# Optimization experiments

Measured on AMD Instinct MI355X. Metric: run time of the kernel, lower is better.

## Reference

```python
import jax, jax.numpy as jnp
import numpy as np

# Complete 32-ary tree of depth 3: vocab = 32**3 = 32768 leaves.
B = 4096       # batch
NHID = 512     # hidden size
BR = 32        # branching factor (num_children at every internal node)
DEPTH = 3      # number of internal-node decisions from root to leaf
V = BR ** DEPTH
NUM_NODES = sum(BR ** k for k in range(DEPTH))  # 1 + 32 + 1024 = 1057

# Static tree-indexing tables (level-order node numbering).
_LEVEL_OFFSET = np.array([sum(BR ** j for j in range(k)) for k in range(DEPTH)], dtype=np.int64)   # [0, 1, 33]
_NODE_DIV = np.array([BR ** (DEPTH - k) for k in range(DEPTH)], dtype=np.int64)                    # node-within-level divisor
_STEP_DIV = np.array([BR ** (DEPTH - 1 - k) for k in range(DEPTH)], dtype=np.int64)                # child-step divisor


def setup_inputs() -> dict:
    key = jax.random.key(0)
    k1, k2, k3 = jax.random.split(key, 3)
    inputs = jax.random.normal(k1, (B, NHID), dtype=jnp.float32)
    labels = jax.random.randint(k2, (B,), 0, V)                     # leaf index per sample
    W = jax.random.normal(k3, (NUM_NODES, NHID, BR), dtype=jnp.float32)  # all node params, stacked
    return {"inputs": inputs, "labels": labels, "W": W}


def reference(inputs, labels, W):
    lab = labels[:, None]                                            # [B, 1]
    node_idx = jnp.asarray(_LEVEL_OFFSET)[None, :] + lab // jnp.asarray(_NODE_DIV)[None, :]  # [B, D] node on path
    steps = (lab // jnp.asarray(_STEP_DIV)[None, :]) % BR            # [B, D] child taken at each node
    Wg = W[node_idx]                                                 # [B, D, NHID, BR] gathered path params
    logits = jnp.einsum('bh,bdhc->bdc', inputs, Wg)                  # [B, D, BR]
    p = jax.nn.softmax(logits, axis=-1)
    step_p = jnp.take_along_axis(p, steps[:, :, None], axis=-1)[..., 0]  # [B, D]
    return jnp.prod(step_p, axis=-1)                                 # [B] path probability
```

## Files before the change

### kernel.cpp

```cpp
#include <hip/hip_runtime.h>


#define NHID  512
#define BR    32
#define BATCH 4096
#define NBUCK 1024
#define SMAX  4
#define SCAP  64

__device__ __forceinline__ float dpp_xadd1(float v) {
    int m = __builtin_amdgcn_update_dpp(0, __float_as_int(v), 0xB1, 0xF, 0xF, true);
    return v + __int_as_float(m);
}
__device__ __forceinline__ float dpp_xadd2(float v) {
    int m = __builtin_amdgcn_update_dpp(0, __float_as_int(v), 0x4E, 0xF, 0xF, true);
    return v + __int_as_float(m);
}

#define FMA4(A, xv, wv_) do { \
    (A).x = fmaf((xv), (wv_).x, (A).x); \
    (A).y = fmaf((xv), (wv_).y, (A).y); \
    (A).z = fmaf((xv), (wv_).z, (A).z); \
    (A).w = fmaf((xv), (wv_).w, (A).w); } while (0)

__global__ __launch_bounds__(256, 4) void hsm_fused(
    const float* __restrict__ inputs,
    const int* __restrict__ labels,
    const float* __restrict__ W,
    float* __restrict__ out)
{
    __shared__ float xsT[NHID * SMAX];
    __shared__ float partial[8 * 3 * SMAX * BR];
    __shared__ float pk[3][SMAX];
    __shared__ int   slist[SCAP];
    __shared__ int   scount;

    const int g   = blockIdx.x;
    const int tid = threadIdx.x;

    if (tid == 0) scount = 0;
    __syncthreads();

    #pragma unroll
    for (int r = 0; r < BATCH / 256; ++r) {
        int j = tid + 256 * r;
        int lab = labels[j];
        if ((lab >> 5) == g) {
            int p = atomicAdd(&scount, 1);
            if (p < SCAP) slist[p] = (j << 5) | (lab & 31);
        }
    }
    __syncthreads();
    const int n = min(scount, SCAP);
    if (n == 0) return;

    const int wv   = tid >> 6;
    const int lane = tid & 63;
    const int hsel = lane & 7;
    const int colg = lane >> 3;

    const int node1 = 1 + (g >> 5);
    const int node2 = 33 + g;

    const size_t laneoff = (size_t)wv * 1024 + hsel * 8 + colg;
    const float4* wp0 = (const float4*)W + laneoff;
    const float4* wp1 = (const float4*)(W + (size_t)node1 * (NHID * BR)) + laneoff;
    const float4* wp2 = (const float4*)(W + (size_t)node2 * (NHID * BR)) + laneoff;
    const float4* xs4 = (const float4*)xsT;

    for (int c0 = 0; c0 < n; c0 += SMAX) {
        const int m = min(SMAX, n - c0);

        __syncthreads();
        #pragma unroll
        for (int r = 0; r < 2; ++r) {
            int h = tid + 256 * r;
            float v[SMAX];
            #pragma unroll
            for (int s = 0; s < SMAX; ++s) {
                float x = 0.0f;
                if (s < m) {
                    int sid = slist[c0 + s] >> 5;
                    x = inputs[(size_t)sid * NHID + h];
                }
                v[s] = x;
            }
            ((float4*)xsT)[h] = make_float4(v[0], v[1], v[2], v[3]);
        }
        __syncthreads();

        float4 acc[3][SMAX];
        #pragma unroll
        for (int k = 0; k < 3; ++k)
            #pragma unroll
            for (int s = 0; s < SMAX; ++s) acc[k][s] = make_float4(0, 0, 0, 0);

        #pragma unroll 4
        for (int i = 0; i < 16; ++i) {
            float4 w0 = wp0[i * 64];
            float4 w1 = wp1[i * 64];
            float4 w2 = wp2[i * 64];
            float4 x4 = xs4[wv * 128 + i * 8 + hsel];
            FMA4(acc[0][0], x4.x, w0); FMA4(acc[0][1], x4.y, w0);
            FMA4(acc[0][2], x4.z, w0); FMA4(acc[0][3], x4.w, w0);
            FMA4(acc[1][0], x4.x, w1); FMA4(acc[1][1], x4.y, w1);
            FMA4(acc[1][2], x4.z, w1); FMA4(acc[1][3], x4.w, w1);
            FMA4(acc[2][0], x4.x, w2); FMA4(acc[2][1], x4.y, w2);
            FMA4(acc[2][2], x4.z, w2); FMA4(acc[2][3], x4.w, w2);
        }

        #pragma unroll
        for (int k = 0; k < 3; ++k) {
            #pragma unroll
            for (int s = 0; s < SMAX; ++s) {
                acc[k][s].x = dpp_xadd2(dpp_xadd1(acc[k][s].x));
                acc[k][s].y = dpp_xadd2(dpp_xadd1(acc[k][s].y));
                acc[k][s].z = dpp_xadd2(dpp_xadd1(acc[k][s].z));
                acc[k][s].w = dpp_xadd2(dpp_xadd1(acc[k][s].w));
            }
        }
        if ((lane & 3) == 0) {
            int wq = wv * 2 + ((lane >> 2) & 1);
            #pragma unroll
            for (int k = 0; k < 3; ++k)
                #pragma unroll
                for (int s = 0; s < SMAX; ++s)
                    *(float4*)&partial[((wq * 3 + k) * SMAX + s) * BR + colg * 4]
                        = acc[k][s];
        }
        __syncthreads();

        if (tid < 32 * SMAX) {
            int s   = tid >> 5;
            int col = tid & 31;
            #pragma unroll
            for (int k = 0; k < 3; ++k) {
                float l = 0.0f;
                #pragma unroll
                for (int wq = 0; wq < 8; ++wq)
                    l += partial[((wq * 3 + k) * SMAX + s) * BR + col];
                float mx = l;
                #pragma unroll
                for (int mm = 1; mm <= 16; mm <<= 1)
                    mx = fmaxf(mx, __shfl_xor(mx, mm));
                float e = expf(l - mx);
                float es = e;
                #pragma unroll
                for (int mm = 1; mm <= 16; mm <<= 1)
                    es += __shfl_xor(es, mm);
                int step = (k == 0) ? (g >> 5)
                         : (k == 1) ? (g & 31)
                                    : (slist[c0 + s] & 31);
                if (col == step) pk[k][s] = e / es;
            }
        }
        __syncthreads();

        if (tid < m) {
            int sid = slist[c0 + tid] >> 5;
            out[sid] = pk[0][tid] * pk[1][tid] * pk[2][tid];
        }
    }
}

extern "C" void kernel_launch(void* const* d_in, const int* in_sizes, int n_in,
                              void* d_out, int out_size, void* d_ws, size_t ws_size,
                              hipStream_t stream)
{
    const float* inputs = (const float*)d_in[0];
    const int*   labels = (const int*)d_in[1];
    const float* W      = (const float*)d_in[2];
    float* out = (float*)d_out;

    hsm_fused<<<dim3(NBUCK), dim3(256), 0, stream>>>(inputs, labels, W, out);
}
```

Measured before the change: 150.5 us.

## Split into label-sort pre-pass and per-group kernel with eight samples per block

Adds a single-block counting-sort kernel that buckets samples by their level-2 node and emits group descriptors of up to eight samples. The main kernel then runs one block per group instead of one per bucket, so blocks no longer each scan all 4096 labels and buckets are no longer looped over in chunks of four. Each block now handles eight samples per weight load, with four waves splitting the hidden dimension and a shuffle-based reduction replacing the DPP one. The cost is an extra serial launch of a single-block sort with many barriers, plus higher register pressure from the doubled accumulators.

```diff
diff --git a/kernel.cpp b/kernel.cpp
--- a/kernel.cpp
+++ b/kernel.cpp
@@ -5,17 +5,8 @@
 #define BR    32
 #define BATCH 4096
 #define NBUCK 1024
-#define SMAX  4
-#define SCAP  64
-
-__device__ __forceinline__ float dpp_xadd1(float v) {
-    int m = __builtin_amdgcn_update_dpp(0, __float_as_int(v), 0xB1, 0xF, 0xF, true);
-    return v + __int_as_float(m);
-}
-__device__ __forceinline__ float dpp_xadd2(float v) {
-    int m = __builtin_amdgcn_update_dpp(0, __float_as_int(v), 0x4E, 0xF, 0xF, true);
-    return v + __int_as_float(m);
-}
+#define GMAX  2048
+#define SMAX  8
 
 #define FMA4(A, xv, wv_) do { \
     (A).x = fmaf((xv), (wv_).x, (A).x); \
@@ -23,143 +14,197 @@
     (A).z = fmaf((xv), (wv_).z, (A).z); \
     (A).w = fmaf((xv), (wv_).w, (A).w); } while (0)
 
-__global__ __launch_bounds__(256, 4) void hsm_fused(
+__global__ __launch_bounds__(1024) void k_sort(const int* __restrict__ labels,
+                                               int* __restrict__ order,
+                                               int* __restrict__ ngroups,
+                                               int* __restrict__ gdesc) {
+    __shared__ int labs[BATCH];
+    __shared__ int hist[NBUCK];
+    __shared__ int scn[NBUCK];
+    __shared__ int desc[GMAX];
+    __shared__ int ng;
+    const int t = threadIdx.x;
+
+    if (t == 0) ng = 0;
+    hist[t] = 0;
+    #pragma unroll
+    for (int r = 0; r < BATCH / 1024; ++r)
+        labs[t + 1024 * r] = labels[t + 1024 * r];
+    __syncthreads();
+    #pragma unroll
+    for (int r = 0; r < BATCH / 1024; ++r)
+        atomicAdd(&hist[labs[t + 1024 * r] >> 5], 1);
+    __syncthreads();
+
+    const int cnt = hist[t];
+    scn[t] = cnt;
+    __syncthreads();
+    for (int d = 1; d < NBUCK; d <<= 1) {
+        int u = (t >= d) ? scn[t - d] : 0;
+        __syncthreads();
+        scn[t] += u;
+        __syncthreads();
+    }
+    const int off = scn[t] - cnt;
+    hist[t] = off;
+
+    for (int j = 0; j < cnt; j += SMAX) {
+        int p = atomicAdd(&ng, 1);
+        desc[p] = (off + j) | (min(SMAX, cnt - j) << 12) | (t << 16);
+    }
+    __syncthreads();
+
+    #pragma unroll
+    for (int r = 0; r < BATCH / 1024; ++r) {
+        int j = t + 1024 * r;
+        int pos = atomicAdd(&hist[labs[j] >> 5], 1);
+        order[pos] = j;
+    }
+    const int n = ng;
+    if (t == 0) *ngroups = n;
+    for (int p = t; p < n; p += 1024) gdesc[p] = desc[p];
+}
+
+__global__ __launch_bounds__(256) void hsm_groups(
     const float* __restrict__ inputs,
     const int* __restrict__ labels,
     const float* __restrict__ W,
+    const int* __restrict__ order,
+    const int* __restrict__ ngroups,
+    const int* __restrict__ gdesc,
     float* __restrict__ out)
 {
-    __shared__ float xsT[NHID * SMAX];
-    __shared__ float partial[8 * 3 * SMAX * BR];
+    __shared__ float xsA[NHID * 4];
+    __shared__ float xsB[NHID * 4];
+    __shared__ float partial[4 * 3 * SMAX * BR];
     __shared__ float pk[3][SMAX];
-    __shared__ int   slist[SCAP];
-    __shared__ int   scount;
-
-    const int g   = blockIdx.x;
-    const int tid = threadIdx.x;
-
-    if (tid == 0) scount = 0;
-    __syncthreads();
-
-    #pragma unroll
-    for (int r = 0; r < BATCH / 256; ++r) {
-        int j = tid + 256 * r;
-        int lab = labels[j];
-        if ((lab >> 5) == g) {
-            int p = atomicAdd(&scount, 1);
-            if (p < SCAP) slist[p] = (j << 5) | (lab & 31);
+    __shared__ int   sids[SMAX];
+    __shared__ int   slab[SMAX];
+
+    const int gid = blockIdx.x;
+    if (gid >= *ngroups) return;
+    const int d     = gdesc[gid];
+    const int start = d & 0xFFF;
+    const int m     = (d >> 12) & 0xF;
+    const int g     = d >> 16;
+    const int tid   = threadIdx.x;
+
+    if (tid < SMAX) {
+        int sid = (tid < m) ? order[start + tid] : -1;
+        sids[tid] = sid;
+        slab[tid] = (sid >= 0) ? labels[sid] : 0;
+    }
+    __syncthreads();
+
+    #pragma unroll
+    for (int r = 0; r < 2; ++r) {
+        int h = tid + 256 * r;
+        float va[4], vb[4];
+        #pragma unroll
+        for (int s = 0; s < 4; ++s) {
+            int ida = sids[s];
+            int idb = sids[s + 4];
+            va[s] = (ida >= 0) ? inputs[(size_t)ida * NHID + h] : 0.0f;
+            vb[s] = (idb >= 0) ? inputs[(size_t)idb * NHID + h] : 0.0f;
         }
-    }
-    __syncthreads();
-    const int n = min(scount, SCAP);
-    if (n == 0) return;
-
-    const int wv   = tid >> 6;
+        ((float4*)xsA)[h] = make_float4(va[0], va[1], va[2], va[3]);
+        ((float4*)xsB)[h] = make_float4(vb[0], vb[1], vb[2], vb[3]);
+    }
+    __syncthreads();
+
+    const int q    = tid >> 6;
     const int lane = tid & 63;
-    const int hsel = lane & 7;
-    const int colg = lane >> 3;
+    const int colg = lane & 7;
+    const int hsel = lane >> 3;
 
     const int node1 = 1 + (g >> 5);
     const int node2 = 33 + g;
 
-    const size_t laneoff = (size_t)wv * 1024 + hsel * 8 + colg;
+    const size_t laneoff = (size_t)q * 1024 + (size_t)hsel * 8 + colg;
     const float4* wp0 = (const float4*)W + laneoff;
     const float4* wp1 = (const float4*)(W + (size_t)node1 * (NHID * BR)) + laneoff;
     const float4* wp2 = (const float4*)(W + (size_t)node2 * (NHID * BR)) + laneoff;
-    const float4* xs4 = (const float4*)xsT;
-
-    for (int c0 = 0; c0 < n; c0 += SMAX) {
-        const int m = min(SMAX, n - c0);
-
-        __syncthreads();
-        #pragma unroll
-        for (int r = 0; r < 2; ++r) {
-            int h = tid + 256 * r;
-            float v[SMAX];
-            #pragma unroll
-            for (int s = 0; s < SMAX; ++s) {
-                float x = 0.0f;
-                if (s < m) {
-                    int sid = slist[c0 + s] >> 5;
-                    x = inputs[(size_t)sid * NHID + h];
-                }
-                v[s] = x;
-            }
-            ((float4*)xsT)[h] = make_float4(v[0], v[1], v[2], v[3]);
-        }
-        __syncthreads();
-
-        float4 acc[3][SMAX];
-        #pragma unroll
-        for (int k = 0; k < 3; ++k)
-            #pragma unroll
-            for (int s = 0; s < SMAX; ++s) acc[k][s] = make_float4(0, 0, 0, 0);
-
-        #pragma unroll 4
-        for (int i = 0; i < 16; ++i) {
-            float4 w0 = wp0[i * 64];
-            float4 w1 = wp1[i * 64];
-            float4 w2 = wp2[i * 64];
-            float4 x4 = xs4[wv * 128 + i * 8 + hsel];
-            FMA4(acc[0][0], x4.x, w0); FMA4(acc[0][1], x4.y, w0);
-            FMA4(acc[0][2], x4.z, w0); FMA4(acc[0][3], x4.w, w0);
-            FMA4(acc[1][0], x4.x, w1); FMA4(acc[1][1], x4.y, w1);
-            FMA4(acc[1][2], x4.z, w1); FMA4(acc[1][3], x4.w, w1);
-            FMA4(acc[2][0], x4.x, w2); FMA4(acc[2][1], x4.y, w2);
-            FMA4(acc[2][2], x4.z, w2); FMA4(acc[2][3], x4.w, w2);
-        }
-
-        #pragma unroll
-        for (int k = 0; k < 3; ++k) {
-            #pragma unroll
-            for (int s = 0; s < SMAX; ++s) {
-                acc[k][s].x = dpp_xadd2(dpp_xadd1(acc[k][s].x));
-                acc[k][s].y = dpp_xadd2(dpp_xadd1(acc[k][s].y));
-                acc[k][s].z = dpp_xadd2(dpp_xadd1(acc[k][s].z));
-                acc[k][s].w = dpp_xadd2(dpp_xadd1(acc[k][s].w));
+    const float4* xa4 = (const float4*)xsA + q * 128 + hsel;
+    const float4* xb4 = (const float4*)xsB + q * 128 + hsel;
+
+    float4 acc[3][SMAX];
+    #pragma unroll
+    for (int k = 0; k < 3; ++k)
+        #pragma unroll
+        for (int s = 0; s < SMAX; ++s) acc[k][s] = make_float4(0, 0, 0, 0);
+
+    #pragma unroll 8
+    for (int i = 0; i < 16; ++i) {
+        float4 w0 = wp0[i * 64];
+        float4 w1 = wp1[i * 64];
+        float4 w2 = wp2[i * 64];
+        float4 xa = xa4[i * 8];
+        float4 xb = xb4[i * 8];
+        FMA4(acc[0][0], xa.x, w0); FMA4(acc[0][1], xa.y, w0);
+        FMA4(acc[0][2], xa.z, w0); FMA4(acc[0][3], xa.w, w0);
+        FMA4(acc[0][4], xb.x, w0); FMA4(acc[0][5], xb.y, w0);
+        FMA4(acc[0][6], xb.z, w0); FMA4(acc[0][7], xb.w, w0);
+        FMA4(acc[1][0], xa.x, w1); FMA4(acc[1][1], xa.y, w1);
+        FMA4(acc[1][2], xa.z, w1); FMA4(acc[1][3], xa.w, w1);
+        FMA4(acc[1][4], xb.x, w1); FMA4(acc[1][5], xb.y, w1);
+        FMA4(acc[1][6], xb.z, w1); FMA4(acc[1][7], xb.w, w1);
+        FMA4(acc[2][0], xa.x, w2); FMA4(acc[2][1], xa.y, w2);
+        FMA4(acc[2][2], xa.z, w2); FMA4(acc[2][3], xa.w, w2);
+        FMA4(acc[2][4], xb.x, w2); FMA4(acc[2][5], xb.y, w2);
+        FMA4(acc[2][6], xb.z, w2); FMA4(acc[2][7], xb.w, w2);
+    }
+
+    #pragma unroll
+    for (int k = 0; k < 3; ++k) {
+        #pragma unroll
+        for (int s = 0; s < SMAX; ++s) {
+            #pragma unroll
+            for (int mm = 8; mm <= 32; mm <<= 1) {
+                acc[k][s].x += __shfl_xor(acc[k][s].x, mm);
+                acc[k][s].y += __shfl_xor(acc[k][s].y, mm);
+                acc[k][s].z += __shfl_xor(acc[k][s].z, mm);
+                acc[k][s].w += __shfl_xor(acc[k][s].w, mm);
             }
         }
-        if ((lane & 3) == 0) {
-            int wq = wv * 2 + ((lane >> 2) & 1);
-            #pragma unroll
-            for (int k = 0; k < 3; ++k)
-                #pragma unroll
-                for (int s = 0; s < SMAX; ++s)
-                    *(float4*)&partial[((wq * 3 + k) * SMAX + s) * BR + colg * 4]
-                        = acc[k][s];
+    }
+    if (lane < 8) {
+        #pragma unroll
+        for (int k = 0; k < 3; ++k)
+            #pragma unroll
+            for (int s = 0; s < SMAX; ++s)
+                *(float4*)&partial[(((q * 3) + k) * SMAX + s) * BR + lane * 4]
+                    = acc[k][s];
+    }
+    __syncthreads();
+
+    {
+        int s   = tid >> 5;
+        int col = tid & 31;
+        #pragma unroll
+        for (int k = 0; k < 3; ++k) {
+            float l = 0.0f;
+            #pragma unroll
+            for (int qq = 0; qq < 4; ++qq)
+                l += partial[(((qq * 3) + k) * SMAX + s) * BR + col];
+            float mx = l;
+            #pragma unroll
+            for (int mm = 1; mm <= 16; mm <<= 1)
+                mx = fmaxf(mx, __shfl_xor(mx, mm));
+            float e  = expf(l - mx);
+            float es = e;
+            #pragma unroll
+            for (int mm = 1; mm <= 16; mm <<= 1)
+                es += __shfl_xor(es, mm);
+            int step = (k == 0) ? (g >> 5)
+                     : (k == 1) ? (g & 31)
+                                : (slab[s] & 31);
+            if (col == step) pk[k][s] = e / es;
         }
-        __syncthreads();
-
-        if (tid < 32 * SMAX) {
-            int s   = tid >> 5;
-            int col = tid & 31;
-            #pragma unroll
-            for (int k = 0; k < 3; ++k) {
-                float l = 0.0f;
-                #pragma unroll
-                for (int wq = 0; wq < 8; ++wq)
-                    l += partial[((wq * 3 + k) * SMAX + s) * BR + col];
-                float mx = l;
-                #pragma unroll
-                for (int mm = 1; mm <= 16; mm <<= 1)
-                    mx = fmaxf(mx, __shfl_xor(mx, mm));
-                float e = expf(l - mx);
-                float es = e;
-                #pragma unroll
-                for (int mm = 1; mm <= 16; mm <<= 1)
-                    es += __shfl_xor(es, mm);
-                int step = (k == 0) ? (g >> 5)
-                         : (k == 1) ? (g & 31)
-                                    : (slist[c0 + s] & 31);
-                if (col == step) pk[k][s] = e / es;
-            }
-        }
-        __syncthreads();
-
-        if (tid < m) {
-            int sid = slist[c0 + tid] >> 5;
-            out[sid] = pk[0][tid] * pk[1][tid] * pk[2][tid];
-        }
+    }
+    __syncthreads();
+
+    if (tid < m) {
+        out[sids[tid]] = pk[0][tid] * pk[1][tid] * pk[2][tid];
     }
 }
 
@@ -172,5 +217,12 @@
     const float* W      = (const float*)d_in[2];
     float* out = (float*)d_out;
 
-    hsm_fused<<<dim3(NBUCK), dim3(256), 0, stream>>>(inputs, labels, W, out);
+    char* ws = (char*)d_ws;
+    int* order   = (int*)ws;
+    int* ngroups = (int*)(ws + 16384);
+    int* gdesc   = (int*)(ws + 16384 + 128);
+
+    k_sort    <<<dim3(1),    dim3(1024), 0, stream>>>(labels, order, ngroups, gdesc);
+    hsm_groups<<<dim3(GMAX), dim3(256),  0, stream>>>(inputs, labels, W, order,
+                                                      ngroups, gdesc, out);
 }
```

Result: faster. 145.0 us (-3.7%).
